# Kernel optimization log

Measured on AMD Instinct MI355X. Metric: run time of the kernel, lower is better.

## Reference

```python
import jax, jax.numpy as jnp
import numpy as np

R_MAX = 2.0
DR_MIN = 0.02
N_ATOMS = 200000
N_EDGES = 12800000

def setup_inputs() -> dict:
    key = jax.random.key(0)
    k1, k2, k3, k4, k5, k6 = jax.random.split(key, 6)
    R = jax.random.normal(k1, (N_ATOMS, 3), dtype=jnp.float32)
    dr_vec = jax.random.normal(k2, (N_EDGES, 3), dtype=jnp.float32)
    Z = jax.random.randint(k3, (N_ATOMS,), 0, 119, dtype=jnp.int32)
    idx = jax.random.randint(k4, (2, N_EDGES), 0, N_ATOMS, dtype=jnp.int32)
    box = jnp.zeros((3, 3), dtype=jnp.float32)
    rep_scale = jax.random.uniform(k5, (119,), dtype=jnp.float32, minval=0.2, maxval=1.8)
    rep_prefactor = jax.random.uniform(k6, (119,), dtype=jnp.float32, minval=0.5, maxval=2.0)
    return {"R": R, "dr_vec": dr_vec, "Z": Z, "idx": idx, "box": box,
            "properties": 0, "rep_scale": rep_scale, "rep_prefactor": rep_prefactor}

def reference(R, dr_vec, Z, idx, box, properties, rep_scale, rep_prefactor):
    idx_i, idx_j = idx[0], idx[1]
    # gather per-edge atomic numbers, then per-element parameters
    Z_i = Z[idx_i]
    Z_j = Z[idx_j]
    # per-edge distance, clipped to [0.02, r_max]
    dr = jnp.sqrt(jnp.sum(dr_vec * dr_vec, axis=-1)).astype(jnp.float32)
    dr = jnp.clip(dr, 0.02, R_MAX)
    cos_cutoff = 0.5 * (jnp.cos(np.pi * dr / R_MAX) + 1.0)
    A_i = jnp.abs(rep_prefactor[Z_i])
    A_j = jnp.abs(rep_prefactor[Z_j])
    R_i = jnp.abs(rep_scale[Z_i])
    R_j = jnp.abs(rep_scale[Z_j])
    f = A_i * A_j * jnp.exp(-dr * (R_i + R_j) / (R_i * R_j)) / (dr * dr)
    E_ij = f * cos_cutoff
    # mask padding/self edges (apax pads neighbor lists with idx_i == idx_j)
    mask = (idx_i != idx_j).astype(E_ij.dtype)
    E_ij = E_ij * mask
    # fp64_sum in original; high-precision accumulation via plain sum here
    E = jnp.sum(E_ij)
    return E
```

## Files before the change

### kernel.cpp

```cpp
#include <hip/hip_runtime.h>
#include <hip/hip_bf16.h>

#define RMAXF 2.0f
#define PI_F 3.14159265358979f

__global__ __launch_bounds__(256) void build_params(
    const int*   __restrict__ Z,
    const float* __restrict__ rep_scale,
    const float* __restrict__ rep_prefactor,
    float2*      __restrict__ par,
    int n_atoms)
{
    int a = blockIdx.x * blockDim.x + threadIdx.x;
    if (a < n_atoms) {
        int z = Z[a];
        float A = fabsf(rep_prefactor[z]);
        float S = __builtin_amdgcn_rcpf(fabsf(rep_scale[z]));
        par[a] = make_float2(A, S);
    }
}

__global__ __launch_bounds__(256) void edge_kernel(
    const float4* __restrict__ dr4,
    const int4*   __restrict__ idx_i4,
    const int4*   __restrict__ idx_j4,
    const float2* __restrict__ par,
    float*        __restrict__ out,
    int n_quads, int n_edges)
{
    int q = blockIdx.x * blockDim.x + threadIdx.x;
    float acc = 0.0f;

    if (q < n_quads) {
        float4 a = dr4[3 * q + 0];
        float4 b = dr4[3 * q + 1];
        float4 c = dr4[3 * q + 2];
        int4 i4 = idx_i4[q];
        int4 j4 = idx_j4[q];

        int ii[4] = { i4.x, i4.y, i4.z, i4.w };
        int jj[4] = { j4.x, j4.y, j4.z, j4.w };

        float2 pi_[4], pj_[4];
        #pragma unroll
        for (int k = 0; k < 4; ++k) { pi_[k] = par[ii[k]]; pj_[k] = par[jj[k]]; }

        float d2[4];
        d2[0] = a.x * a.x + a.y * a.y + a.z * a.z;
        d2[1] = a.w * a.w + b.x * b.x + b.y * b.y;
        d2[2] = b.z * b.z + b.w * b.w + c.x * c.x;
        d2[3] = c.y * c.y + c.z * c.z + c.w * c.w;

        #pragma unroll
        for (int k = 0; k < 4; ++k) {
            float d2c = fminf(fmaxf(d2[k], 4.0e-4f), 4.0f);
            float dr  = __builtin_amdgcn_sqrtf(d2c);
            float cv  = __cosf((0.25f * PI_F) * dr);
            float e   = __expf(-dr * (pi_[k].y + pj_[k].y));
            float f   = pi_[k].x * pj_[k].x * e * __builtin_amdgcn_rcpf(d2c) * cv * cv;
            acc += (ii[k] != jj[k]) ? f : 0.0f;
        }
    }

    if (blockIdx.x == gridDim.x - 1 && threadIdx.x == 0) {
        const float* drf = (const float*)dr4;
        const int* idx_i = (const int*)idx_i4;
        const int* idx_j = (const int*)idx_j4;
        for (int e = n_quads * 4; e < n_edges; ++e) {
            float x = drf[3 * e + 0], y = drf[3 * e + 1], z = drf[3 * e + 2];
            float d2c = fminf(fmaxf(x * x + y * y + z * z, 4.0e-4f), 4.0f);
            float dr  = sqrtf(d2c);
            float cv  = __cosf((0.25f * PI_F) * dr);
            int i = idx_i[e], j = idx_j[e];
            float2 pi_ = par[i], pj_ = par[j];
            float f = pi_.x * pj_.x * __expf(-dr * (pi_.y + pj_.y)) / d2c * cv * cv;
            if (i != j) acc += f;
        }
    }

    #pragma unroll
    for (int off = 32; off > 0; off >>= 1)
        acc += __shfl_down(acc, off, 64);

    __shared__ float wsum[4];
    int lane = threadIdx.x & 63;
    int wid  = threadIdx.x >> 6;
    if (lane == 0) wsum[wid] = acc;
    __syncthreads();
    if (threadIdx.x == 0)
        atomicAdd(out, wsum[0] + wsum[1] + wsum[2] + wsum[3]);
}

__global__ __launch_bounds__(256) void edge_kernel_fallback(
    const float* __restrict__ drf,
    const int*   __restrict__ idx_i,
    const int*   __restrict__ idx_j,
    const int*   __restrict__ Z,
    const float* __restrict__ rep_scale,
    const float* __restrict__ rep_prefactor,
    float*       __restrict__ out,
    int n_edges)
{
    __shared__ float2 tab[128];
    for (int t = threadIdx.x; t < 119; t += blockDim.x)
        tab[t] = make_float2(fabsf(rep_prefactor[t]),
                             __builtin_amdgcn_rcpf(fabsf(rep_scale[t])));
    __syncthreads();

    float acc = 0.0f;
    const int stride = gridDim.x * blockDim.x;
    for (int e = blockIdx.x * blockDim.x + threadIdx.x; e < n_edges; e += stride) {
        float x = drf[3 * e + 0], y = drf[3 * e + 1], z = drf[3 * e + 2];
        float d2c = fminf(fmaxf(x * x + y * y + z * z, 4.0e-4f), 4.0f);
        float dr  = __builtin_amdgcn_sqrtf(d2c);
        float cv  = __cosf((0.25f * PI_F) * dr);
        int i = idx_i[e], j = idx_j[e];
        float2 pi_ = tab[Z[i]], pj_ = tab[Z[j]];
        float f = pi_.x * pj_.x * __expf(-dr * (pi_.y + pj_.y))
                  * __builtin_amdgcn_rcpf(d2c) * cv * cv;
        acc += (i != j) ? f : 0.0f;
    }

    #pragma unroll
    for (int off = 32; off > 0; off >>= 1)
        acc += __shfl_down(acc, off, 64);
    __shared__ float wsum[4];
    int lane = threadIdx.x & 63;
    int wid  = threadIdx.x >> 6;
    if (lane == 0) wsum[wid] = acc;
    __syncthreads();
    if (threadIdx.x == 0)
        atomicAdd(out, wsum[0] + wsum[1] + wsum[2] + wsum[3]);
}

extern "C" void kernel_launch(void* const* d_in, const int* in_sizes, int n_in,
                              void* d_out, int out_size, void* d_ws, size_t ws_size,
                              hipStream_t stream) {
    const float* dr_vec        = (const float*)d_in[1];
    const int*   Z             = (const int*)d_in[2];
    const int*   idx           = (const int*)d_in[3];
    const float* rep_scale     = (const float*)d_in[6];
    const float* rep_prefactor = (const float*)d_in[7];
    float* out = (float*)d_out;

    const int n_atoms = in_sizes[2];
    const int n_edges = in_sizes[3] / 2;
    const int n_quads = n_edges / 4;
    const int* idx_i = idx;
    const int* idx_j = idx + n_edges;

    hipMemsetAsync(d_out, 0, sizeof(float), stream);

    const size_t par_bytes = (size_t)n_atoms * sizeof(float2);
    const bool aligned = ((n_edges & 3) == 0);

    if (ws_size >= par_bytes && aligned) {
        float2* par = (float2*)d_ws;
        build_params<<<(n_atoms + 255) / 256, 256, 0, stream>>>(
            Z, rep_scale, rep_prefactor, par, n_atoms);
        edge_kernel<<<(n_quads + 255) / 256, 256, 0, stream>>>(
            (const float4*)dr_vec, (const int4*)idx_i, (const int4*)idx_j,
            par, out, n_quads, n_edges);
    } else {
        int blocks = (n_edges + 255) / 256;
        if (blocks > 4096) blocks = 4096;
        edge_kernel_fallback<<<blocks, 256, 0, stream>>>(
            dr_vec, idx_i, idx_j, Z, rep_scale, rep_prefactor, out, n_edges);
    }
}
```

Baseline: 385.3 us.

## Pack per-atom params as half2, process 8 edges per thread with nontemporal loads

```diff
diff --git a/kernel.cpp b/kernel.cpp
--- a/kernel.cpp
+++ b/kernel.cpp
@@ -1,63 +1,78 @@
 #include <hip/hip_runtime.h>
 #include <hip/hip_bf16.h>
+#include <hip/hip_fp16.h>
 
 #define RMAXF 2.0f
 #define PI_F 3.14159265358979f
+
+typedef float f32x4 __attribute__((ext_vector_type(4)));
+typedef int   i32x4 __attribute__((ext_vector_type(4)));
 
 __global__ __launch_bounds__(256) void build_params(
     const int*   __restrict__ Z,
     const float* __restrict__ rep_scale,
     const float* __restrict__ rep_prefactor,
-    float2*      __restrict__ par,
+    __half2*     __restrict__ parh,
     int n_atoms)
 {
     int a = blockIdx.x * blockDim.x + threadIdx.x;
     if (a < n_atoms) {
         int z = Z[a];
         float A = fabsf(rep_prefactor[z]);
-        float S = __builtin_amdgcn_rcpf(fabsf(rep_scale[z]));
-        par[a] = make_float2(A, S);
+        float S = 1.0f / fabsf(rep_scale[z]);
+        parh[a] = __floats2half2_rn(A, S);
     }
 }
 
 __global__ __launch_bounds__(256) void edge_kernel(
-    const float4* __restrict__ dr4,
-    const int4*   __restrict__ idx_i4,
-    const int4*   __restrict__ idx_j4,
-    const float2* __restrict__ par,
+    const f32x4* __restrict__ dr4,
+    const i32x4* __restrict__ idx_i4,
+    const i32x4* __restrict__ idx_j4,
+    const __half2* __restrict__ parh,
     float*        __restrict__ out,
-    int n_quads, int n_edges)
+    int n_oct, int n_edges)
 {
     int q = blockIdx.x * blockDim.x + threadIdx.x;
     float acc = 0.0f;
 
-    if (q < n_quads) {
-        float4 a = dr4[3 * q + 0];
-        float4 b = dr4[3 * q + 1];
-        float4 c = dr4[3 * q + 2];
-        int4 i4 = idx_i4[q];
-        int4 j4 = idx_j4[q];
+    if (q < n_oct) {
+        f32x4 va = __builtin_nontemporal_load(&dr4[6 * q + 0]);
+        f32x4 vb = __builtin_nontemporal_load(&dr4[6 * q + 1]);
+        f32x4 vc = __builtin_nontemporal_load(&dr4[6 * q + 2]);
+        f32x4 vd = __builtin_nontemporal_load(&dr4[6 * q + 3]);
+        f32x4 ve = __builtin_nontemporal_load(&dr4[6 * q + 4]);
+        f32x4 vg = __builtin_nontemporal_load(&dr4[6 * q + 5]);
+        i32x4 ia = __builtin_nontemporal_load(&idx_i4[2 * q + 0]);
+        i32x4 ib = __builtin_nontemporal_load(&idx_i4[2 * q + 1]);
+        i32x4 ja = __builtin_nontemporal_load(&idx_j4[2 * q + 0]);
+        i32x4 jb = __builtin_nontemporal_load(&idx_j4[2 * q + 1]);
 
-        int ii[4] = { i4.x, i4.y, i4.z, i4.w };
-        int jj[4] = { j4.x, j4.y, j4.z, j4.w };
+        int ii[8] = { ia.x, ia.y, ia.z, ia.w, ib.x, ib.y, ib.z, ib.w };
+        int jj[8] = { ja.x, ja.y, ja.z, ja.w, jb.x, jb.y, jb.z, jb.w };
 
-        float2 pi_[4], pj_[4];
+        __half2 hi[8], hj[8];
         #pragma unroll
-        for (int k = 0; k < 4; ++k) { pi_[k] = par[ii[k]]; pj_[k] = par[jj[k]]; }
+        for (int k = 0; k < 8; ++k) { hi[k] = parh[ii[k]]; hj[k] = parh[jj[k]]; }
 
-        float d2[4];
-        d2[0] = a.x * a.x + a.y * a.y + a.z * a.z;
-        d2[1] = a.w * a.w + b.x * b.x + b.y * b.y;
-        d2[2] = b.z * b.z + b.w * b.w + c.x * c.x;
-        d2[3] = c.y * c.y + c.z * c.z + c.w * c.w;
+        float d2[8];
+        d2[0] = va.x * va.x + va.y * va.y + va.z * va.z;
+        d2[1] = va.w * va.w + vb.x * vb.x + vb.y * vb.y;
+        d2[2] = vb.z * vb.z + vb.w * vb.w + vc.x * vc.x;
+        d2[3] = vc.y * vc.y + vc.z * vc.z + vc.w * vc.w;
+        d2[4] = vd.x * vd.x + vd.y * vd.y + vd.z * vd.z;
+        d2[5] = vd.w * vd.w + ve.x * ve.x + ve.y * ve.y;
+        d2[6] = ve.z * ve.z + ve.w * ve.w + vg.x * vg.x;
+        d2[7] = vg.y * vg.y + vg.z * vg.z + vg.w * vg.w;
 
         #pragma unroll
-        for (int k = 0; k < 4; ++k) {
+        for (int k = 0; k < 8; ++k) {
+            float2 pi_ = __half22float2(hi[k]);
+            float2 pj_ = __half22float2(hj[k]);
             float d2c = fminf(fmaxf(d2[k], 4.0e-4f), 4.0f);
             float dr  = __builtin_amdgcn_sqrtf(d2c);
             float cv  = __cosf((0.25f * PI_F) * dr);
-            float e   = __expf(-dr * (pi_[k].y + pj_[k].y));
-            float f   = pi_[k].x * pj_[k].x * e * __builtin_amdgcn_rcpf(d2c) * cv * cv;
+            float e   = __expf(-dr * (pi_.y + pj_.y));
+            float f   = pi_.x * pj_.x * e * __builtin_amdgcn_rcpf(d2c) * cv * cv;
             acc += (ii[k] != jj[k]) ? f : 0.0f;
         }
     }
@@ -66,13 +81,14 @@
         const float* drf = (const float*)dr4;
         const int* idx_i = (const int*)idx_i4;
         const int* idx_j = (const int*)idx_j4;
-        for (int e = n_quads * 4; e < n_edges; ++e) {
+        for (int e = n_oct * 8; e < n_edges; ++e) {
             float x = drf[3 * e + 0], y = drf[3 * e + 1], z = drf[3 * e + 2];
             float d2c = fminf(fmaxf(x * x + y * y + z * z, 4.0e-4f), 4.0f);
             float dr  = sqrtf(d2c);
             float cv  = __cosf((0.25f * PI_F) * dr);
             int i = idx_i[e], j = idx_j[e];
-            float2 pi_ = par[i], pj_ = par[j];
+            float2 pi_ = __half22float2(parh[i]);
+            float2 pj_ = __half22float2(parh[j]);
             float f = pi_.x * pj_.x * __expf(-dr * (pi_.y + pj_.y)) / d2c * cv * cv;
             if (i != j) acc += f;
         }
@@ -104,7 +120,7 @@
     __shared__ float2 tab[128];
     for (int t = threadIdx.x; t < 119; t += blockDim.x)
         tab[t] = make_float2(fabsf(rep_prefactor[t]),
-                             __builtin_amdgcn_rcpf(fabsf(rep_scale[t])));
+                             1.0f / fabsf(rep_scale[t]));
     __syncthreads();
 
     float acc = 0.0f;
@@ -145,22 +161,22 @@
 
     const int n_atoms = in_sizes[2];
     const int n_edges = in_sizes[3] / 2;
-    const int n_quads = n_edges / 4;
+    const int n_oct   = n_edges / 8;
     const int* idx_i = idx;
     const int* idx_j = idx + n_edges;
 
-    hipMemsetAsync(d_out, 0, sizeof(float), stream);
+    (void)hipMemsetAsync(d_out, 0, sizeof(float), stream);
 
-    const size_t par_bytes = (size_t)n_atoms * sizeof(float2);
-    const bool aligned = ((n_edges & 3) == 0);
+    const size_t par_bytes = (size_t)n_atoms * sizeof(__half2);
+    const bool aligned = ((n_edges & 7) == 0);
 
     if (ws_size >= par_bytes && aligned) {
-        float2* par = (float2*)d_ws;
+        __half2* parh = (__half2*)d_ws;
         build_params<<<(n_atoms + 255) / 256, 256, 0, stream>>>(
-            Z, rep_scale, rep_prefactor, par, n_atoms);
-        edge_kernel<<<(n_quads + 255) / 256, 256, 0, stream>>>(
-            (const float4*)dr_vec, (const int4*)idx_i, (const int4*)idx_j,
-            par, out, n_quads, n_edges);
+            Z, rep_scale, rep_prefactor, parh, n_atoms);
+        edge_kernel<<<(n_oct + 255) / 256, 256, 0, stream>>>(
+            (const f32x4*)dr_vec, (const i32x4*)idx_i, (const i32x4*)idx_j,
+            parh, out, n_oct, n_edges);
     } else {
         int blocks = (n_edges + 255) / 256;
         if (blocks > 4096) blocks = 4096;
```

Result: slower. 393.5 us (+2.1%).
